# Kernel optimization log

Hardware: AMD Instinct MI355X
Metric: run time of the kernel (lower is better)

Reference implementation:

```python
import jax, jax.numpy as jnp
import numpy as np

N = 100_000      # nodes
E = 1_600_000    # edges (avg degree 16)
IN_DIM = 128
HID = 512
NCLS = 64
BN_EPS = 1e-5


def setup_inputs() -> dict:
    key = jax.random.key(0)
    ks = jax.random.split(key, 16)

    def lin(k, fi, fo):
        kw, kb = jax.random.split(k)
        s = 1.0 / np.sqrt(fi)
        return (jax.random.uniform(kw, (fi, fo), jnp.float32, -s, s),
                jax.random.uniform(kb, (fo,), jnp.float32, -s, s))

    W1a, b1a = lin(ks[2], IN_DIM, HID)
    W1b, b1b = lin(ks[3], HID, HID)
    W2a, b2a = lin(ks[4], HID, HID)
    W2b, b2b = lin(ks[5], HID, NCLS)
    return {
        "x": jax.random.normal(ks[0], (N, IN_DIM), jnp.float32),
        "edge_index": jax.random.randint(ks[1], (2, E), 0, N, jnp.int32),
        "g": jnp.zeros((1,), jnp.int32),
        "A_k": jnp.zeros((1,), jnp.int32),
        "D": jnp.zeros((1,), jnp.int32),
        "Kindices": jnp.zeros((1,), jnp.int32),
        "de": jnp.zeros((1,), jnp.int32),
        "M": jnp.zeros((1,), jnp.int32),
        "I": jnp.zeros((1,), jnp.int32),
        "W1a": W1a, "b1a": b1a, "W1b": W1b, "b1b": b1b,
        "gamma1": jnp.ones((HID,), jnp.float32), "beta1": jnp.zeros((HID,), jnp.float32),
        "W2a": W2a, "b2a": b2a, "W2b": W2b, "b2b": b2b,
        "gamma2": jnp.ones((NCLS,), jnp.float32), "beta2": jnp.zeros((NCLS,), jnp.float32),
    }


def _gin_conv(x, src, dst, Wa, ba, Wb, bb):
    # PyG GINConv (eps=0): nn(x + sum_{j in N(i)} x_j); messages x[src] summed at dst
    agg = jax.ops.segment_sum(x[src], dst, num_segments=N)
    h = x + agg
    h = jax.nn.relu(h @ Wa + ba)
    return h @ Wb + bb


def _batchnorm(x, gamma, beta):
    # training-mode BatchNorm1d: batch stats over node dim, biased variance
    mu = jnp.mean(x, axis=0)
    var = jnp.mean(jnp.square(x - mu), axis=0)
    return gamma * (x - mu) * jax.lax.rsqrt(var + BN_EPS) + beta


def reference(x, edge_index, g, A_k, D, Kindices, de, M, I,
              W1a, b1a, W1b, b1b, gamma1, beta1,
              W2a, b2a, W2b, b2b, gamma2, beta2):
    src, dst = edge_index[0], edge_index[1]
    h = jax.nn.selu(_gin_conv(x, src, dst, W1a, b1a, W1b, b1b))
    h = _batchnorm(h, gamma1, beta1)
    # dropout(p=0.5) omitted (eval-mode / deterministic reference)
    h = jax.nn.selu(_gin_conv(h, src, dst, W2a, b2a, W2b, b2b))
    h = _batchnorm(h, gamma2, beta2)
    return jax.nn.softmax(h, axis=1)
```

## Files before the change

kernel.cpp:

```cpp
#include <hip/hip_runtime.h>
#include <hip/hip_bf16.h>

#define N_NODES 100000
#define N_EDGES 1600000
#define IN_DIM 128
#define HID 512
#define NCLS 64

typedef __attribute__((ext_vector_type(8))) short bf16x8;
typedef __attribute__((ext_vector_type(4))) float f32x4;

#define RB_COUNT 782
#define RB_PAD 784
#define TG_GRID (RB_PAD * 4)

__device__ inline float bf2f(unsigned short b) {
    unsigned int u = ((unsigned int)b) << 16;
    return __builtin_bit_cast(float, u);
}
__device__ inline unsigned short f2bf(float f) {
    unsigned int u = __builtin_bit_cast(unsigned int, f);
    unsigned int lsb = (u >> 16) & 1u;
    u += 0x7fffu + lsb;
    return (unsigned short)(u >> 16);
}
__device__ inline float selu_f(float x) {
    const float scale = 1.0507009873554805f;
    const float alpha = 1.6732632423543772f;
    return x > 0.f ? scale * x : scale * alpha * (__expf(x) - 1.f);
}
__device__ inline void stb(float* p, float v) { *p = v; }
__device__ inline void stb(unsigned short* p, float v) { *p = f2bf(v); }

__device__ inline void gl_lds16(const void* g, void* l) {
    __builtin_amdgcn_global_load_lds((const __attribute__((address_space(1))) void*)g,
                                     (__attribute__((address_space(3))) void*)l, 16, 0, 0);
}

__global__ __launch_bounds__(256) void k_cast(const float* __restrict__ x,
                                              unsigned short* __restrict__ xb) {
    size_t g = (size_t)blockIdx.x * 256 + threadIdx.x;
    size_t total = (size_t)N_NODES * IN_DIM / 8;
    if (g >= total) return;
    const float4* p = (const float4*)(x + g * 8);
    float4 v0 = p[0], v1 = p[1];
    uint4 o;
    o.x = (unsigned)f2bf(v0.x) | ((unsigned)f2bf(v0.y) << 16);
    o.y = (unsigned)f2bf(v0.z) | ((unsigned)f2bf(v0.w) << 16);
    o.z = (unsigned)f2bf(v1.x) | ((unsigned)f2bf(v1.y) << 16);
    o.w = (unsigned)f2bf(v1.z) | ((unsigned)f2bf(v1.w) << 16);
    ((uint4*)xb)[g] = o;
}

__global__ __launch_bounds__(256) void k_deg(const int* __restrict__ dst, int* __restrict__ deg) {
    int e = blockIdx.x * 256 + threadIdx.x;
    if (e < N_EDGES) atomicAdd(&deg[dst[e]], 1);
}

#define SCAN_NB 98

__global__ __launch_bounds__(256) void k_scan_part(const int* __restrict__ deg, int* __restrict__ part) {
    __shared__ int sd[256];
    int b = blockIdx.x, t = threadIdx.x;
    int i0 = b * 1024 + t * 4;
    int s = 0;
#pragma unroll
    for (int k = 0; k < 4; ++k) if (i0 + k < N_NODES) s += deg[i0 + k];
    sd[t] = s;
    __syncthreads();
    for (int o = 128; o > 0; o >>= 1) {
        if (t < o) sd[t] += sd[t + o];
        __syncthreads();
    }
    if (t == 0) part[b] = sd[0];
}

__global__ __launch_bounds__(128) void k_scan_mid(const int* __restrict__ part, int* __restrict__ base,
                                                  int* __restrict__ off) {
    __shared__ int sp[128];
    int t = threadIdx.x;
    int v = (t < SCAN_NB) ? part[t] : 0;
    sp[t] = v;
    __syncthreads();
    for (int o = 1; o < 128; o <<= 1) {
        int tv = (t >= o) ? sp[t - o] : 0;
        __syncthreads();
        sp[t] += tv;
        __syncthreads();
    }
    if (t < SCAN_NB) base[t] = sp[t] - v;
    if (t == SCAN_NB - 1) off[N_NODES] = sp[t];
}

__global__ __launch_bounds__(256) void k_scan_fin(const int* __restrict__ deg, const int* __restrict__ base,
                                                  int* __restrict__ off, int* __restrict__ pos) {
    __shared__ int sd[256];
    int b = blockIdx.x, t = threadIdx.x;
    int i0 = b * 1024 + t * 4;
    int v[4]; int s = 0;
#pragma unroll
    for (int k = 0; k < 4; ++k) { v[k] = (i0 + k < N_NODES) ? deg[i0 + k] : 0; s += v[k]; }
    sd[t] = s;
    __syncthreads();
    for (int o = 1; o < 256; o <<= 1) {
        int tv = (t >= o) ? sd[t - o] : 0;
        __syncthreads();
        sd[t] += tv;
        __syncthreads();
    }
    int excl = base[b] + sd[t] - s;
#pragma unroll
    for (int k = 0; k < 4; ++k) {
        if (i0 + k < N_NODES) { off[i0 + k] = excl; pos[i0 + k] = excl; excl += v[k]; }
    }
}

__global__ __launch_bounds__(256) void k_fill(const int* __restrict__ src, const int* __restrict__ dst,
                                              int* __restrict__ pos, int* __restrict__ adj) {
    int e = blockIdx.x * 256 + threadIdx.x;
    if (e < N_EDGES) {
        int p = atomicAdd(&pos[dst[e]], 1);
        adj[p] = src[e];
    }
}

__global__ __launch_bounds__(256) void k_sortadj(const int* __restrict__ off, int* __restrict__ adj) {
    __shared__ int sb[64 * 256];
    int n = blockIdx.x * 256 + threadIdx.x;
    if (n >= N_NODES) return;
    int t = threadIdx.x;
    int e0 = off[n], e1 = off[n + 1];
    int d = e1 - e0;
    if (d <= 1 || d > 64) return;
    for (int i = 0; i < d; ++i) sb[i * 256 + t] = adj[e0 + i];
    for (int i = 1; i < d; ++i) {
        int key = sb[i * 256 + t];
        int j = i - 1;
        while (j >= 0 && sb[j * 256 + t] > key) {
            sb[(j + 1) * 256 + t] = sb[j * 256 + t];
            --j;
        }
        sb[(j + 1) * 256 + t] = key;
    }
    for (int i = 0; i < d; ++i) adj[e0 + i] = sb[i * 256 + t];
}

__global__ __launch_bounds__(256) void k_pack(const float* __restrict__ W,
                                              unsigned short* __restrict__ Wp, int K, int NC) {
    int idx = blockIdx.x * 256 + threadIdx.x;
    if (idx >= K * NC) return;
    int j = idx & 7;
    int l = (idx >> 3) & 63;
    int t = idx >> 9;
    int KT = K >> 5;
    int kt = t % KT;
    int nt = t / KT;
    int k = kt * 32 + (l >> 4) * 8 + j;
    int n = nt * 16 + (l & 15);
    Wp[idx] = f2bf(W[(size_t)k * NC + n]);
}

__global__ __launch_bounds__(256) void k_packT(const float* __restrict__ W,
                                               unsigned short* __restrict__ WT, int K, int NC) {
    int idx = blockIdx.x * 256 + threadIdx.x;
    if (idx >= K * NC) return;
    int k = idx & (K - 1);
    int n = idx / K;
    WT[idx] = f2bf(W[(size_t)k * NC + n]);
}

__global__ __launch_bounds__(256) void k_agg1(const unsigned short* __restrict__ xb,
                                              const int* __restrict__ off, const int* __restrict__ adj,
                                              unsigned short* __restrict__ A1) {
    int w = (blockIdx.x * 256 + threadIdx.x) >> 6;
    if (w >= N_NODES) return;
    int lane = threadIdx.x & 63;
    unsigned v = ((const unsigned*)(xb + (size_t)w * IN_DIM))[lane];
    float s0 = bf2f((unsigned short)(v & 0xffff));
    float s1 = bf2f((unsigned short)(v >> 16));
    int e0 = off[w], e1 = off[w + 1];
    int e = e0;
    for (; e + 4 <= e1; e += 4) {
        int j0 = adj[e], j1 = adj[e + 1], j2 = adj[e + 2], j3 = adj[e + 3];
        unsigned u0 = ((const unsigned*)(xb + (size_t)j0 * IN_DIM))[lane];
        unsigned u1 = ((const unsigned*)(xb + (size_t)j1 * IN_DIM))[lane];
        unsigned u2 = ((const unsigned*)(xb + (size_t)j2 * IN_DIM))[lane];
        unsigned u3 = ((const unsigned*)(xb + (size_t)j3 * IN_DIM))[lane];
        s0 += bf2f((unsigned short)(u0 & 0xffff)) + bf2f((unsigned short)(u1 & 0xffff)) +
              bf2f((unsigned short)(u2 & 0xffff)) + bf2f((unsigned short)(u3 & 0xffff));
        s1 += bf2f((unsigned short)(u0 >> 16)) + bf2f((unsigned short)(u1 >> 16)) +
              bf2f((unsigned short)(u2 >> 16)) + bf2f((unsigned short)(u3 >> 16));
    }
    for (; e < e1; ++e) {
        unsigned u = ((const unsigned*)(xb + (size_t)adj[e] * IN_DIM))[lane];
        s0 += bf2f((unsigned short)(u & 0xffff));
        s1 += bf2f((unsigned short)(u >> 16));
    }
    ((unsigned*)(A1 + (size_t)w * IN_DIM))[lane] = (unsigned)f2bf(s0) | ((unsigned)f2bf(s1) << 16);
}

__global__ __launch_bounds__(256) void k_aggbn2(const unsigned short* __restrict__ h,
                                                const int* __restrict__ off, const int* __restrict__ adj,
                                                const float* __restrict__ bn,
                                                unsigned short* __restrict__ outb) {
    int w = (blockIdx.x * 256 + threadIdx.x) >> 6;
    if (w >= N_NODES) return;
    int lane = threadIdx.x & 63;
    int fb = blockIdx.y * 256 + lane * 4;
    const unsigned short* hp = h + fb;
    float scl[4], shf[4];
#pragma unroll
    for (int k = 0; k < 4; ++k) {
        scl[k] = bn[2 * HID + fb + k];
        shf[k] = bn[3 * HID + fb + k];
    }
    uint2 v = *(const uint2*)(hp + (size_t)w * HID);
    float s0 = bf2f((unsigned short)(v.x & 0xffff));
    float s1 = bf2f((unsigned short)(v.x >> 16));
    float s2 = bf2f((unsigned short)(v.y & 0xffff));
    float s3 = bf2f((unsigned short)(v.y >> 16));
    int e0 = off[w], e1 = off[w + 1];
    int e = e0;
    for (; e + 4 <= e1; e += 4) {
        int j0 = adj[e], j1 = adj[e + 1], j2 = adj[e + 2], j3 = adj[e + 3];
        uint2 u0 = *(const uint2*)(hp + (size_t)j0 * HID);
        uint2 u1 = *(const uint2*)(hp + (size_t)j1 * HID);
        uint2 u2 = *(const uint2*)(hp + (size_t)j2 * HID);
        uint2 u3 = *(const uint2*)(hp + (size_t)j3 * HID);
        s0 += bf2f((unsigned short)(u0.x & 0xffff)) + bf2f((unsigned short)(u1.x & 0xffff)) +
              bf2f((unsigned short)(u2.x & 0xffff)) + bf2f((unsigned short)(u3.x & 0xffff));
        s1 += bf2f((unsigned short)(u0.x >> 16)) + bf2f((unsigned short)(u1.x >> 16)) +
              bf2f((unsigned short)(u2.x >> 16)) + bf2f((unsigned short)(u3.x >> 16));
        s2 += bf2f((unsigned short)(u0.y & 0xffff)) + bf2f((unsigned short)(u1.y & 0xffff)) +
              bf2f((unsigned short)(u2.y & 0xffff)) + bf2f((unsigned short)(u3.y & 0xffff));
        s3 += bf2f((unsigned short)(u0.y >> 16)) + bf2f((unsigned short)(u1.y >> 16)) +
              bf2f((unsigned short)(u2.y >> 16)) + bf2f((unsigned short)(u3.y >> 16));
    }
    for (; e < e1; ++e) {
        uint2 u = *(const uint2*)(hp + (size_t)adj[e] * HID);
        s0 += bf2f((unsigned short)(u.x & 0xffff));
        s1 += bf2f((unsigned short)(u.x >> 16));
        s2 += bf2f((unsigned short)(u.y & 0xffff));
        s3 += bf2f((unsigned short)(u.y >> 16));
    }
    float dp1 = (float)(e1 - e0 + 1);
    float r0 = s0 * scl[0] + dp1 * shf[0];
    float r1 = s1 * scl[1] + dp1 * shf[1];
    float r2 = s2 * scl[2] + dp1 * shf[2];
    float r3 = s3 * scl[3] + dp1 * shf[3];
    unsigned long long o =
        (unsigned long long)((unsigned)f2bf(r0) | ((unsigned)f2bf(r1) << 16)) |
        ((unsigned long long)((unsigned)f2bf(r2) | ((unsigned)f2bf(r3) << 16)) << 32);
    __builtin_nontemporal_store(o, (unsigned long long*)(outb + (size_t)w * HID + fb));
}

template <int K, int ACT, int STATS>
__global__ __launch_bounds__(256) void k_tgemm(const unsigned short* __restrict__ A,
                                               const unsigned short* __restrict__ WT,
                                               const float* __restrict__ bias,
                                               unsigned short* __restrict__ Out,
                                               float* __restrict__ scratch, int M) {
    constexpr int NC = 512;
    __shared__ __align__(16) char smem[32768 + 2048];
    const int bid = blockIdx.x;
    const int r8 = bid & 7;
    const int q = bid >> 3;
    const int cb = q & 3;
    const int rb = (q >> 2) * 8 + r8;
    const int rowbase = rb * 128;
    const int colbase = cb * 128;
    if (rowbase >= M) return;

    const int tid = threadIdx.x;
    const int lane = tid & 63;
    const int w = tid >> 6;
    const int wm = w >> 1, wn = w & 1;
    const int l15 = lane & 15, lg = lane >> 4;

    f32x4 acc[4][4];
#pragma unroll
    for (int i = 0; i < 4; ++i)
#pragma unroll
        for (int j = 0; j < 4; ++j) acc[i][j] = (f32x4)0.f;

    for (int k0 = 0; k0 < K; k0 += 64) {
#pragma unroll
        for (int i = 0; i < 4; ++i) {
            int slot = i * 256 + tid;
            int r = slot >> 3;
            int u = (slot & 7) ^ (r & 7);
            int gr = rowbase + r; if (gr >= M) gr = M - 1;
            gl_lds16(A + (size_t)gr * K + k0 + u * 8, smem + (i * 256 + w * 64) * 16);
        }
#pragma unroll
        for (int i = 0; i < 4; ++i) {
            int slot = i * 256 + tid;
            int c = slot >> 3;
            int u = (slot & 7) ^ (c & 7);
            gl_lds16(WT + (size_t)(colbase + c) * K + k0 + u * 8,
                     smem + 16384 + (i * 256 + w * 64) * 16);
        }
        __syncthreads();
#pragma unroll
        for (int kin = 0; kin < 2; ++kin) {
            bf16x8 af[4], bfr[4];
#pragma unroll
            for (int mi = 0; mi < 4; ++mi) {
                int r = wm * 64 + mi * 16 + l15;
                int u = (kin * 4 + lg) ^ (r & 7);
                af[mi] = *(const bf16x8*)(smem + r * 128 + u * 16);
            }
#pragma unroll
            for (int ni = 0; ni < 4; ++ni) {
                int c = wn * 64 + ni * 16 + l15;
                int u = (kin * 4 + lg) ^ (c & 7);
                bfr[ni] = *(const bf16x8*)(smem + 16384 + c * 128 + u * 16);
            }
#pragma unroll
            for (int mi = 0; mi < 4; ++mi)
#pragma unroll
                for (int ni = 0; ni < 4; ++ni)
                    acc[mi][ni] = __builtin_amdgcn_mfma_f32_16x16x32_bf16(af[mi], bfr[ni], acc[mi][ni], 0, 0, 0);
        }
        __syncthreads();
    }

    float cs[4], cq[4];
    if (STATS) {
#pragma unroll
        for (int ni = 0; ni < 4; ++ni) { cs[ni] = 0.f; cq[ni] = 0.f; }
    }
#pragma unroll
    for (int ni = 0; ni < 4; ++ni) {
        int c = wn * 64 + ni * 16 + l15;
        float bv = bias[colbase + c];
#pragma unroll
        for (int mi = 0; mi < 4; ++mi) {
#pragma unroll
            for (int r = 0; r < 4; ++r) {
                int row = wm * 64 + mi * 16 + lg * 4 + r;
                float t = acc[mi][ni][r] + bv;
                t = (ACT == 0) ? fmaxf(t, 0.f) : selu_f(t);
                if (STATS && (rowbase + row < M)) { cs[ni] += t; cq[ni] += t * t; }
                int byte = (row * 256 + c * 2) ^ ((row & 7) << 4);
                *(unsigned short*)(smem + byte) = f2bf(t);
            }
        }
    }
    if (STATS) {
        float* sS = (float*)(smem + 32768);
#pragma unroll
        for (int ni = 0; ni < 4; ++ni) {
            float a = cs[ni];
            a += __shfl_xor(a, 16); a += __shfl_xor(a, 32);
            float b = cq[ni];
            b += __shfl_xor(b, 16); b += __shfl_xor(b, 32);
            if (lg == 0) {
                sS[wm * 256 + (wn * 64 + ni * 16 + l15)] = a;
                sS[wm * 256 + 128 + (wn * 64 + ni * 16 + l15)] = b;
            }
        }
    }
    __syncthreads();
#pragma unroll
    for (int it = 0; it < 8; ++it) {
        int idx = it * 256 + tid;
        int row = idx >> 4;
        int ch = idx & 15;
        int gr = rowbase + row;
        if (gr < M) {
            uint4 v = *(const uint4*)(smem + row * 256 + ((ch ^ (row & 7)) << 4));
            *(uint4*)(Out + (size_t)gr * NC + colbase + ch * 8) = v;
        }
    }
    if (STATS) {
        const float* sS = (const float*)(smem + 32768);
        int c = tid & 127, kind = tid >> 7;
        float v = sS[kind * 128 + c] + sS[256 + kind * 128 + c];
        scratch[(size_t)(rb * 4 + cb) * 256 + kind * 128 + c] = v;
    }
}

__global__ __launch_bounds__(256) void k_bnred(const float* __restrict__ scratch,
                                               float* __restrict__ bn) {
    int t = threadIdx.x;
    float loc[4] = {0.f, 0.f, 0.f, 0.f};
    for (int rb = blockIdx.x; rb < RB_COUNT; rb += gridDim.x) {
#pragma unroll
        for (int cbk = 0; cbk < 4; ++cbk)
            loc[cbk] += scratch[(size_t)(rb * 4 + cbk) * 256 + t];
    }
    int kind = t >> 7, cl = t & 127;
#pragma unroll
    for (int cbk = 0; cbk < 4; ++cbk)
        atomicAdd(&bn[kind * HID + cbk * 128 + cl], loc[cbk]);
}

template <int K, int NC, int ACT, int WAVES_M, int WAVES_N, int NFRAG, int STATS, typename TOUT>
__global__ __launch_bounds__(WAVES_M * WAVES_N * 64) void k_mgemm(
    const unsigned short* __restrict__ A, const unsigned short* __restrict__ Wp,
    const float* __restrict__ bias, TOUT* __restrict__ Out, float* __restrict__ bnacc, int M) {
    __shared__ float sS[WAVES_M * WAVES_N * 128];
    const int tid = threadIdx.x;
    const int lane = tid & 63;
    const int w = tid >> 6;
    const int wm = w / WAVES_N;
    const int wn = w % WAVES_N;
    const int l15 = lane & 15;
    const int lg = lane >> 4;
    const int rowbase = blockIdx.x * (32 * WAVES_M) + wm * 32;
    const int colbase = blockIdx.y * (WAVES_N * 16 * NFRAG) + wn * 16 * NFRAG;
    int r0 = rowbase + l15; if (r0 > M - 1) r0 = M - 1;
    int r1 = rowbase + 16 + l15; if (r1 > M - 1) r1 = M - 1;
    const unsigned short* pa0 = A + (size_t)r0 * K + lg * 8;
    const unsigned short* pa1 = A + (size_t)r1 * K + lg * 8;
    const unsigned short* pw = Wp + (size_t)(colbase >> 4) * (K / 32) * 512 + lane * 8;

    f32x4 acc[2][NFRAG];
#pragma unroll
    for (int i = 0; i < 2; ++i)
#pragma unroll
        for (int j = 0; j < NFRAG; ++j) acc[i][j] = (f32x4)0.f;

#pragma unroll 2
    for (int kt = 0; kt < K / 32; ++kt) {
        bf16x8 a0 = *(const bf16x8*)(pa0 + kt * 32);
        bf16x8 a1 = *(const bf16x8*)(pa1 + kt * 32);
#pragma unroll
        for (int ni = 0; ni < NFRAG; ++ni) {
            bf16x8 bv = *(const bf16x8*)(pw + (ni * (K / 32) + kt) * 512);
            acc[0][ni] = __builtin_amdgcn_mfma_f32_16x16x32_bf16(a0, bv, acc[0][ni], 0, 0, 0);
            acc[1][ni] = __builtin_amdgcn_mfma_f32_16x16x32_bf16(a1, bv, acc[1][ni], 0, 0, 0);
        }
    }

    float cs[NFRAG], cq[NFRAG];
    if (STATS) {
#pragma unroll
        for (int ni = 0; ni < NFRAG; ++ni) { cs[ni] = 0.f; cq[ni] = 0.f; }
    }
#pragma unroll
    for (int ni = 0; ni < NFRAG; ++ni) {
        int c = colbase + ni * 16 + l15;
        float bv = bias[c];
#pragma unroll
        for (int mi = 0; mi < 2; ++mi) {
#pragma unroll
            for (int r = 0; r < 4; ++r) {
                int row = rowbase + mi * 16 + lg * 4 + r;
                if (row < M) {
                    float t = acc[mi][ni][r] + bv;
                    t = (ACT == 0) ? fmaxf(t, 0.f) : selu_f(t);
                    if (STATS) { cs[ni] += t; cq[ni] += t * t; }
                    stb(&Out[(size_t)row * NC + c], t);
                }
            }
        }
    }
    if (STATS) {
#pragma unroll
        for (int ni = 0; ni < NFRAG; ++ni) {
            float a = cs[ni];
            a += __shfl_xor(a, 16); a += __shfl_xor(a, 32);
            float b = cq[ni];
            b += __shfl_xor(b, 16); b += __shfl_xor(b, 32);
            if (lg == 0) {
                sS[w * 128 + (ni * 16 + l15)] = a;
                sS[w * 128 + 64 + (ni * 16 + l15)] = b;
            }
        }
        __syncthreads();
        if (tid < 128) {
            float v = 0.f;
#pragma unroll
            for (int ww = 0; ww < WAVES_M * WAVES_N; ++ww) v += sS[ww * 128 + tid];
            atomicAdd(&bnacc[tid], v);
        }
    }
}

__global__ void k_bnprep(float* __restrict__ bn, const float* __restrict__ gamma,
                         const float* __restrict__ beta, int C, float invn) {
    int c = threadIdx.x + blockIdx.x * blockDim.x;
    if (c >= C) return;
    float mu = bn[c] * invn;
    float var = bn[C + c] * invn - mu * mu;
    float sc = gamma[c] * rsqrtf(var + 1e-5f);
    bn[2 * C + c] = sc;
    bn[3 * C + c] = beta[c] - mu * sc;
}

__global__ __launch_bounds__(256) void k_softmax(float* __restrict__ O, const float* __restrict__ bn2) {
    int w = (blockIdx.x * 256 + threadIdx.x) >> 6;
    if (w >= N_NODES) return;
    int lane = threadIdx.x & 63;
    float z = O[(size_t)w * NCLS + lane] * bn2[2 * NCLS + lane] + bn2[3 * NCLS + lane];
    float m = z;
#pragma unroll
    for (int o = 32; o > 0; o >>= 1) m = fmaxf(m, __shfl_xor(m, o));
    float e = __expf(z - m);
    float s = e;
#pragma unroll
    for (int o = 32; o > 0; o >>= 1) s += __shfl_xor(s, o);
    O[(size_t)w * NCLS + lane] = e / s;
}

extern "C" void kernel_launch(void* const* d_in, const int* in_sizes, int n_in,
                              void* d_out, int out_size, void* d_ws, size_t ws_size,
                              hipStream_t stream) {
    const float* x = (const float*)d_in[0];
    const int* edge = (const int*)d_in[1];
    const int* srcp = edge;
    const int* dstp = edge + N_EDGES;
    const float* W1a = (const float*)d_in[9];
    const float* b1a = (const float*)d_in[10];
    const float* W1b = (const float*)d_in[11];
    const float* b1b = (const float*)d_in[12];
    const float* gamma1 = (const float*)d_in[13];
    const float* beta1 = (const float*)d_in[14];
    const float* W2a = (const float*)d_in[15];
    const float* b2a = (const float*)d_in[16];
    const float* W2b = (const float*)d_in[17];
    const float* b2b = (const float*)d_in[18];
    const float* gamma2 = (const float*)d_in[19];
    const float* beta2 = (const float*)d_in[20];
    float* out = (float*)d_out;

    char* ws = (char*)d_ws;
    size_t o = 0;
    auto alloc = [&](size_t bytes) -> char* {
        char* p = ws + o;
        o = (o + bytes + 255) & ~(size_t)255;
        return p;
    };
    int* off = (int*)alloc((N_NODES + 1) * sizeof(int));
    int* deg = (int*)alloc(N_NODES * sizeof(int));
    int* pos = (int*)alloc(N_NODES * sizeof(int));
    int* adj = (int*)alloc(N_EDGES * sizeof(int));
    int* part = (int*)alloc(SCAN_NB * sizeof(int));
    int* base = (int*)alloc(SCAN_NB * sizeof(int));
    float* bn1 = (float*)alloc(4 * HID * sizeof(float));
    float* bn2 = (float*)alloc(4 * NCLS * sizeof(float));
    float* stat = (float*)alloc((size_t)RB_COUNT * 4 * 256 * sizeof(float));
    unsigned short* WT1 = (unsigned short*)alloc((size_t)IN_DIM * HID * sizeof(unsigned short));
    unsigned short* WT2 = (unsigned short*)alloc((size_t)HID * HID * sizeof(unsigned short));
    unsigned short* WT3 = (unsigned short*)alloc((size_t)HID * HID * sizeof(unsigned short));
    unsigned short* Wp4 = (unsigned short*)alloc((size_t)HID * NCLS * sizeof(unsigned short));
    unsigned short* xb = (unsigned short*)alloc((size_t)N_NODES * IN_DIM * sizeof(unsigned short));
    unsigned short* A1 = (unsigned short*)alloc((size_t)N_NODES * IN_DIM * sizeof(unsigned short));
    unsigned short* B = (unsigned short*)alloc((size_t)N_NODES * HID * sizeof(unsigned short));
    unsigned short* C = (unsigned short*)alloc((size_t)N_NODES * HID * sizeof(unsigned short));

    hipMemsetAsync(deg, 0, N_NODES * sizeof(int), stream);
    hipMemsetAsync(bn1, 0, 2 * HID * sizeof(float), stream);
    hipMemsetAsync(bn2, 0, 2 * NCLS * sizeof(float), stream);

    int eb = (N_EDGES + 255) / 256;
    k_cast<<<(N_NODES * IN_DIM / 8 + 255) / 256, 256, 0, stream>>>(x, xb);
    k_deg<<<eb, 256, 0, stream>>>(dstp, deg);
    k_scan_part<<<SCAN_NB, 256, 0, stream>>>(deg, part);
    k_scan_mid<<<1, 128, 0, stream>>>(part, base, off);
    k_scan_fin<<<SCAN_NB, 256, 0, stream>>>(deg, base, off, pos);
    k_fill<<<eb, 256, 0, stream>>>(srcp, dstp, pos, adj);
    k_sortadj<<<(N_NODES + 255) / 256, 256, 0, stream>>>(off, adj);

    k_packT<<<(IN_DIM * HID) / 256, 256, 0, stream>>>(W1a, WT1, IN_DIM, HID);
    k_packT<<<(HID * HID) / 256, 256, 0, stream>>>(W1b, WT2, HID, HID);
    k_packT<<<(HID * HID) / 256, 256, 0, stream>>>(W2a, WT3, HID, HID);
    k_pack<<<(HID * NCLS) / 256, 256, 0, stream>>>(W2b, Wp4, HID, NCLS);

    int nwb = (N_NODES * 64 + 255) / 256;

    k_agg1<<<nwb, 256, 0, stream>>>(xb, off, adj, A1);
    k_tgemm<IN_DIM, 0, 0><<<TG_GRID, 256, 0, stream>>>(A1, WT1, b1a, B, nullptr, N_NODES);
    k_tgemm<HID, 1, 1><<<TG_GRID, 256, 0, stream>>>(B, WT2, b1b, C, stat, N_NODES);
    k_bnred<<<32, 256, 0, stream>>>(stat, bn1);
    k_bnprep<<<2, 256, 0, stream>>>(bn1, gamma1, beta1, HID, 1.0f / N_NODES);

    k_aggbn2<<<dim3(nwb, 2), 256, 0, stream>>>(C, off, adj, bn1, B);
    k_tgemm<HID, 0, 0><<<TG_GRID, 256, 0, stream>>>(B, WT3, b2a, C, nullptr, N_NODES);
    k_mgemm<HID, NCLS, 1, 8, 1, 4, 1, float><<<dim3((N_NODES + 255) / 256, 1), 512, 0, stream>>>(C, Wp4, b2b, out, bn2, N_NODES);

    k_bnprep<<<1, 64, 0, stream>>>(bn2, gamma2, beta2, NCLS, 1.0f / N_NODES);
    k_softmax<<<nwb, 256, 0, stream>>>(out, bn2);
}
```

Measured before the change: 881.5 us.

## Split layer-2 aggregation into eight feature slices with edge-parallel lanes

The second-layer gather/BN kernel now handles 64-feature slices across eight sequential launches, with each wavefront's four 16-lane groups splitting a node's edges and reducing through cross-lane shuffles. The intent is to shrink the gathered working set per launch (100k nodes × 64 features in bf16) so that it fits in cache, raising hit rates on the random neighbour reads. The cost is eight launches instead of one, eight re-reads of the CSR offsets and adjacency, and shuffle reductions. Each gather is also narrower (8 bytes per lane across 16 lanes, so 128-byte segments).

After: 1.114 ms. +26.4%, slower.

```diff
diff --git a/kernel.cpp b/kernel.cpp
--- a/kernel.cpp
+++ b/kernel.cpp
@@ -199,59 +199,60 @@
     ((unsigned*)(A1 + (size_t)w * IN_DIM))[lane] = (unsigned)f2bf(s0) | ((unsigned)f2bf(s1) << 16);
 }
 
-__global__ __launch_bounds__(256) void k_aggbn2(const unsigned short* __restrict__ h,
+__global__ __launch_bounds__(256) void k_aggbn8(const unsigned short* __restrict__ h,
                                                 const int* __restrict__ off, const int* __restrict__ adj,
                                                 const float* __restrict__ bn,
-                                                unsigned short* __restrict__ outb) {
+                                                unsigned short* __restrict__ outb, int slice) {
     int w = (blockIdx.x * 256 + threadIdx.x) >> 6;
     if (w >= N_NODES) return;
     int lane = threadIdx.x & 63;
-    int fb = blockIdx.y * 256 + lane * 4;
+    int es = lane >> 4;
+    int fl = lane & 15;
+    int fb = slice * 64 + fl * 4;
     const unsigned short* hp = h + fb;
-    float scl[4], shf[4];
-#pragma unroll
-    for (int k = 0; k < 4; ++k) {
-        scl[k] = bn[2 * HID + fb + k];
-        shf[k] = bn[3 * HID + fb + k];
-    }
-    uint2 v = *(const uint2*)(hp + (size_t)w * HID);
-    float s0 = bf2f((unsigned short)(v.x & 0xffff));
-    float s1 = bf2f((unsigned short)(v.x >> 16));
-    float s2 = bf2f((unsigned short)(v.y & 0xffff));
-    float s3 = bf2f((unsigned short)(v.y >> 16));
+    float s0 = 0.f, s1 = 0.f, s2 = 0.f, s3 = 0.f;
+    if (es == 0) {
+        unsigned long long sv = __builtin_nontemporal_load(
+            (const unsigned long long*)(hp + (size_t)w * HID));
+        s0 = bf2f((unsigned short)(sv & 0xffff));
+        s1 = bf2f((unsigned short)((sv >> 16) & 0xffff));
+        s2 = bf2f((unsigned short)((sv >> 32) & 0xffff));
+        s3 = bf2f((unsigned short)((sv >> 48) & 0xffff));
+    }
     int e0 = off[w], e1 = off[w + 1];
-    int e = e0;
-    for (; e + 4 <= e1; e += 4) {
-        int j0 = adj[e], j1 = adj[e + 1], j2 = adj[e + 2], j3 = adj[e + 3];
-        uint2 u0 = *(const uint2*)(hp + (size_t)j0 * HID);
-        uint2 u1 = *(const uint2*)(hp + (size_t)j1 * HID);
-        uint2 u2 = *(const uint2*)(hp + (size_t)j2 * HID);
-        uint2 u3 = *(const uint2*)(hp + (size_t)j3 * HID);
-        s0 += bf2f((unsigned short)(u0.x & 0xffff)) + bf2f((unsigned short)(u1.x & 0xffff)) +
-              bf2f((unsigned short)(u2.x & 0xffff)) + bf2f((unsigned short)(u3.x & 0xffff));
-        s1 += bf2f((unsigned short)(u0.x >> 16)) + bf2f((unsigned short)(u1.x >> 16)) +
-              bf2f((unsigned short)(u2.x >> 16)) + bf2f((unsigned short)(u3.x >> 16));
-        s2 += bf2f((unsigned short)(u0.y & 0xffff)) + bf2f((unsigned short)(u1.y & 0xffff)) +
-              bf2f((unsigned short)(u2.y & 0xffff)) + bf2f((unsigned short)(u3.y & 0xffff));
-        s3 += bf2f((unsigned short)(u0.y >> 16)) + bf2f((unsigned short)(u1.y >> 16)) +
-              bf2f((unsigned short)(u2.y >> 16)) + bf2f((unsigned short)(u3.y >> 16));
-    }
-    for (; e < e1; ++e) {
-        uint2 u = *(const uint2*)(hp + (size_t)adj[e] * HID);
+    int e = e0 + es;
+    for (; e + 4 < e1; e += 8) {
+        int ja = adj[e], jb = adj[e + 4];
+        uint2 ua = *(const uint2*)(hp + (size_t)ja * HID);
+        uint2 ub = *(const uint2*)(hp + (size_t)jb * HID);
+        s0 += bf2f((unsigned short)(ua.x & 0xffff)) + bf2f((unsigned short)(ub.x & 0xffff));
+        s1 += bf2f((unsigned short)(ua.x >> 16)) + bf2f((unsigned short)(ub.x >> 16));
+        s2 += bf2f((unsigned short)(ua.y & 0xffff)) + bf2f((unsigned short)(ub.y & 0xffff));
+        s3 += bf2f((unsigned short)(ua.y >> 16)) + bf2f((unsigned short)(ub.y >> 16));
+    }
+    for (; e < e1; e += 4) {
+        int j = adj[e];
+        uint2 u = *(const uint2*)(hp + (size_t)j * HID);
         s0 += bf2f((unsigned short)(u.x & 0xffff));
         s1 += bf2f((unsigned short)(u.x >> 16));
         s2 += bf2f((unsigned short)(u.y & 0xffff));
         s3 += bf2f((unsigned short)(u.y >> 16));
     }
-    float dp1 = (float)(e1 - e0 + 1);
-    float r0 = s0 * scl[0] + dp1 * shf[0];
-    float r1 = s1 * scl[1] + dp1 * shf[1];
-    float r2 = s2 * scl[2] + dp1 * shf[2];
-    float r3 = s3 * scl[3] + dp1 * shf[3];
-    unsigned long long o =
-        (unsigned long long)((unsigned)f2bf(r0) | ((unsigned)f2bf(r1) << 16)) |
-        ((unsigned long long)((unsigned)f2bf(r2) | ((unsigned)f2bf(r3) << 16)) << 32);
-    __builtin_nontemporal_store(o, (unsigned long long*)(outb + (size_t)w * HID + fb));
+    s0 += __shfl_xor(s0, 16); s0 += __shfl_xor(s0, 32);
+    s1 += __shfl_xor(s1, 16); s1 += __shfl_xor(s1, 32);
+    s2 += __shfl_xor(s2, 16); s2 += __shfl_xor(s2, 32);
+    s3 += __shfl_xor(s3, 16); s3 += __shfl_xor(s3, 32);
+    if (es == 0) {
+        float dp1 = (float)(e1 - e0 + 1);
+        float r0 = s0 * bn[2 * HID + fb + 0] + dp1 * bn[3 * HID + fb + 0];
+        float r1 = s1 * bn[2 * HID + fb + 1] + dp1 * bn[3 * HID + fb + 1];
+        float r2 = s2 * bn[2 * HID + fb + 2] + dp1 * bn[3 * HID + fb + 2];
+        float r3 = s3 * bn[2 * HID + fb + 3] + dp1 * bn[3 * HID + fb + 3];
+        unsigned long long o =
+            (unsigned long long)((unsigned)f2bf(r0) | ((unsigned)f2bf(r1) << 16)) |
+            ((unsigned long long)((unsigned)f2bf(r2) | ((unsigned)f2bf(r3) << 16)) << 32);
+        __builtin_nontemporal_store(o, (unsigned long long*)(outb + (size_t)w * HID + fb));
+    }
 }
 
 template <int K, int ACT, int STATS>
@@ -577,8 +578,10 @@
     k_bnred<<<32, 256, 0, stream>>>(stat, bn1);
     k_bnprep<<<2, 256, 0, stream>>>(bn1, gamma1, beta1, HID, 1.0f / N_NODES);
 
-    k_aggbn2<<<dim3(nwb, 2), 256, 0, stream>>>(C, off, adj, bn1, B);
-    k_tgemm<HID, 0, 0><<<TG_GRID, 256, 0, stream>>>(B, WT3, b2a, C, nullptr, N_NODES);
+    for (int sl = 0; sl < 8; ++sl)
+        k_aggbn8<<<nwb, 256, 0, stream>>>(C, off, adj, bn1, B, sl);
+
+    k_tgemm<HID, 0, 0><<<TG_GRID, 256, 0, stream>>>(B, WT3, b2a, C, N_NODES ? nullptr : nullptr, N_NODES);
     k_mgemm<HID, NCLS, 1, 8, 1, 4, 1, float><<<dim3((N_NODES + 255) / 256, 1), 512, 0, stream>>>(C, Wp4, b2b, out, bn2, N_NODES);
 
     k_bnprep<<<1, 64, 0, stream>>>(bn2, gamma2, beta2, NCLS, 1.0f / N_NODES);
```

## Load GEMM weights directly from pre-packed MFMA layout instead of LDS staging

Applied to the files above, without the earlier changes.

The three 512-column GEMMs now read weight fragments straight from global memory in a pre-packed per-lane MFMA layout (k_pack), instead of staging a transposed weight tile through LDS. LDS use is halved, and the epilogue writes the output in two 64-row passes so it fits in the smaller buffer. This removes the weight LDS copy and may raise occupancy. In exchange, each wave issues global or L2 loads for B fragments inside the K loop, which adds latency and redundant traffic across waves, plus extra barriers in the epilogue.

Result: slower. 949.4 us (+7.7%).

```diff
diff --git a/kernel.cpp b/kernel.cpp
--- a/kernel.cpp
+++ b/kernel.cpp
@@ -158,15 +158,6 @@
     int k = kt * 32 + (l >> 4) * 8 + j;
     int n = nt * 16 + (l & 15);
     Wp[idx] = f2bf(W[(size_t)k * NC + n]);
-}
-
-__global__ __launch_bounds__(256) void k_packT(const float* __restrict__ W,
-                                               unsigned short* __restrict__ WT, int K, int NC) {
-    int idx = blockIdx.x * 256 + threadIdx.x;
-    if (idx >= K * NC) return;
-    int k = idx & (K - 1);
-    int n = idx / K;
-    WT[idx] = f2bf(W[(size_t)k * NC + n]);
 }
 
 __global__ __launch_bounds__(256) void k_agg1(const unsigned short* __restrict__ xb,
@@ -255,13 +246,14 @@
 }
 
 template <int K, int ACT, int STATS>
-__global__ __launch_bounds__(256) void k_tgemm(const unsigned short* __restrict__ A,
-                                               const unsigned short* __restrict__ WT,
+__global__ __launch_bounds__(256) void k_hgemm(const unsigned short* __restrict__ A,
+                                               const unsigned short* __restrict__ Wp,
                                                const float* __restrict__ bias,
                                                unsigned short* __restrict__ Out,
                                                float* __restrict__ scratch, int M) {
     constexpr int NC = 512;
-    __shared__ __align__(16) char smem[32768 + 2048];
+    constexpr int KT = K / 32;
+    __shared__ __align__(16) char smem[16384 + 2048];
     const int bid = blockIdx.x;
     const int r8 = bid & 7;
     const int q = bid >> 3;
@@ -276,6 +268,8 @@
     const int w = tid >> 6;
     const int wm = w >> 1, wn = w & 1;
     const int l15 = lane & 15, lg = lane >> 4;
+    const int ntbase = (colbase >> 4) + wn * 4;
+    const unsigned short* pwb = Wp + (size_t)lane * 8;
 
     f32x4 acc[4][4];
 #pragma unroll
@@ -292,18 +286,11 @@
             int gr = rowbase + r; if (gr >= M) gr = M - 1;
             gl_lds16(A + (size_t)gr * K + k0 + u * 8, smem + (i * 256 + w * 64) * 16);
         }
-#pragma unroll
-        for (int i = 0; i < 4; ++i) {
-            int slot = i * 256 + tid;
-            int c = slot >> 3;
-            int u = (slot & 7) ^ (c & 7);
-            gl_lds16(WT + (size_t)(colbase + c) * K + k0 + u * 8,
-                     smem + 16384 + (i * 256 + w * 64) * 16);
-        }
         __syncthreads();
 #pragma unroll
         for (int kin = 0; kin < 2; ++kin) {
-            bf16x8 af[4], bfr[4];
+            int kt = (k0 >> 5) + kin;
+            bf16x8 af[4], bv[4];
 #pragma unroll
             for (int mi = 0; mi < 4; ++mi) {
                 int r = wm * 64 + mi * 16 + l15;
@@ -311,44 +298,59 @@
                 af[mi] = *(const bf16x8*)(smem + r * 128 + u * 16);
             }
 #pragma unroll
+            for (int ni = 0; ni < 4; ++ni)
+                bv[ni] = *(const bf16x8*)(pwb + (size_t)((ntbase + ni) * KT + kt) * 512);
+#pragma unroll
+            for (int ni = 0; ni < 4; ++ni)
+#pragma unroll
+                for (int mi = 0; mi < 4; ++mi)
+                    acc[mi][ni] = __builtin_amdgcn_mfma_f32_16x16x32_bf16(af[mi], bv[ni], acc[mi][ni], 0, 0, 0);
+        }
+        __syncthreads();
+    }
+
+    float cs[4], cq[4];
+    if (STATS) {
+#pragma unroll
+        for (int ni = 0; ni < 4; ++ni) { cs[ni] = 0.f; cq[ni] = 0.f; }
+    }
+#pragma unroll
+    for (int pass = 0; pass < 2; ++pass) {
+        if (wm == pass) {
+#pragma unroll
             for (int ni = 0; ni < 4; ++ni) {
                 int c = wn * 64 + ni * 16 + l15;
-                int u = (kin * 4 + lg) ^ (c & 7);
-                bfr[ni] = *(const bf16x8*)(smem + 16384 + c * 128 + u * 16);
+                float bvs = bias[colbase + c];
+#pragma unroll
+                for (int mi = 0; mi < 4; ++mi) {
+#pragma unroll
+                    for (int r = 0; r < 4; ++r) {
+                        int rloc = mi * 16 + lg * 4 + r;
+                        float t = acc[mi][ni][r] + bvs;
+                        t = (ACT == 0) ? fmaxf(t, 0.f) : selu_f(t);
+                        if (STATS && (rowbase + pass * 64 + rloc < M)) { cs[ni] += t; cq[ni] += t * t; }
+                        int byte = (rloc * 256 + c * 2) ^ ((rloc & 7) << 4);
+                        *(unsigned short*)(smem + byte) = f2bf(t);
+                    }
+                }
             }
-#pragma unroll
-            for (int mi = 0; mi < 4; ++mi)
-#pragma unroll
-                for (int ni = 0; ni < 4; ++ni)
-                    acc[mi][ni] = __builtin_amdgcn_mfma_f32_16x16x32_bf16(af[mi], bfr[ni], acc[mi][ni], 0, 0, 0);
-        }
-        __syncthreads();
-    }
-
-    float cs[4], cq[4];
+        }
+        __syncthreads();
+#pragma unroll
+        for (int it = 0; it < 4; ++it) {
+            int idx = it * 256 + tid;
+            int row = idx >> 4;
+            int ch = idx & 15;
+            int gr = rowbase + pass * 64 + row;
+            if (gr < M) {
+                uint4 v = *(const uint4*)(smem + row * 256 + ((ch ^ (row & 7)) << 4));
+                *(uint4*)(Out + (size_t)gr * NC + colbase + ch * 8) = v;
+            }
+        }
+        __syncthreads();
+    }
     if (STATS) {
-#pragma unroll
-        for (int ni = 0; ni < 4; ++ni) { cs[ni] = 0.f; cq[ni] = 0.f; }
-    }
-#pragma unroll
-    for (int ni = 0; ni < 4; ++ni) {
-        int c = wn * 64 + ni * 16 + l15;
-        float bv = bias[colbase + c];
-#pragma unroll
-        for (int mi = 0; mi < 4; ++mi) {
-#pragma unroll
-            for (int r = 0; r < 4; ++r) {
-                int row = wm * 64 + mi * 16 + lg * 4 + r;
-                float t = acc[mi][ni][r] + bv;
-                t = (ACT == 0) ? fmaxf(t, 0.f) : selu_f(t);
-                if (STATS && (rowbase + row < M)) { cs[ni] += t; cq[ni] += t * t; }
-                int byte = (row * 256 + c * 2) ^ ((row & 7) << 4);
-                *(unsigned short*)(smem + byte) = f2bf(t);
-            }
-        }
-    }
-    if (STATS) {
-        float* sS = (float*)(smem + 32768);
+        float* sS = (float*)(smem + 16384);
 #pragma unroll
         for (int ni = 0; ni < 4; ++ni) {
             float a = cs[ni];
@@ -360,24 +362,12 @@
                 sS[wm * 256 + 128 + (wn * 64 + ni * 16 + l15)] = b;
             }
         }
-    }
-    __syncthreads();
-#pragma unroll
-    for (int it = 0; it < 8; ++it) {
-        int idx = it * 256 + tid;
-        int row = idx >> 4;
-        int ch = idx & 15;
-        int gr = rowbase + row;
-        if (gr < M) {
-            uint4 v = *(const uint4*)(smem + row * 256 + ((ch ^ (row & 7)) << 4));
-            *(uint4*)(Out + (size_t)gr * NC + colbase + ch * 8) = v;
-        }
-    }
-    if (STATS) {
-        const float* sS = (const float*)(smem + 32768);
+        __syncthreads();
         int c = tid & 127, kind = tid >> 7;
-        float v = sS[kind * 128 + c] + sS[256 + kind * 128 + c];
-        scratch[(size_t)(rb * 4 + cb) * 256 + kind * 128 + c] = v;
+        if (tid < 256) {
+            float v = sS[kind * 128 + c] + sS[256 + kind * 128 + c];
+            scratch[(size_t)(rb * 4 + cb) * 256 + kind * 128 + c] = v;
+        }
     }
 }
 
@@ -542,9 +532,9 @@
     float* bn1 = (float*)alloc(4 * HID * sizeof(float));
     float* bn2 = (float*)alloc(4 * NCLS * sizeof(float));
     float* stat = (float*)alloc((size_t)RB_COUNT * 4 * 256 * sizeof(float));
-    unsigned short* WT1 = (unsigned short*)alloc((size_t)IN_DIM * HID * sizeof(unsigned short));
-    unsigned short* WT2 = (unsigned short*)alloc((size_t)HID * HID * sizeof(unsigned short));
-    unsigned short* WT3 = (unsigned short*)alloc((size_t)HID * HID * sizeof(unsigned short));
+    unsigned short* Wp1 = (unsigned short*)alloc((size_t)IN_DIM * HID * sizeof(unsigned short));
+    unsigned short* Wp2 = (unsigned short*)alloc((size_t)HID * HID * sizeof(unsigned short));
+    unsigned short* Wp3 = (unsigned short*)alloc((size_t)HID * HID * sizeof(unsigned short));
     unsigned short* Wp4 = (unsigned short*)alloc((size_t)HID * NCLS * sizeof(unsigned short));
     unsigned short* xb = (unsigned short*)alloc((size_t)N_NODES * IN_DIM * sizeof(unsigned short));
     unsigned short* A1 = (unsigned short*)alloc((size_t)N_NODES * IN_DIM * sizeof(unsigned short));
@@ -564,21 +554,21 @@
     k_fill<<<eb, 256, 0, stream>>>(srcp, dstp, pos, adj);
     k_sortadj<<<(N_NODES + 255) / 256, 256, 0, stream>>>(off, adj);
 
-    k_packT<<<(IN_DIM * HID) / 256, 256, 0, stream>>>(W1a, WT1, IN_DIM, HID);
-    k_packT<<<(HID * HID) / 256, 256, 0, stream>>>(W1b, WT2, HID, HID);
-    k_packT<<<(HID * HID) / 256, 256, 0, stream>>>(W2a, WT3, HID, HID);
+    k_pack<<<(IN_DIM * HID) / 256, 256, 0, stream>>>(W1a, Wp1, IN_DIM, HID);
+    k_pack<<<(HID * HID) / 256, 256, 0, stream>>>(W1b, Wp2, HID, HID);
+    k_pack<<<(HID * HID) / 256, 256, 0, stream>>>(W2a, Wp3, HID, HID);
     k_pack<<<(HID * NCLS) / 256, 256, 0, stream>>>(W2b, Wp4, HID, NCLS);
 
     int nwb = (N_NODES * 64 + 255) / 256;
 
     k_agg1<<<nwb, 256, 0, stream>>>(xb, off, adj, A1);
-    k_tgemm<IN_DIM, 0, 0><<<TG_GRID, 256, 0, stream>>>(A1, WT1, b1a, B, nullptr, N_NODES);
-    k_tgemm<HID, 1, 1><<<TG_GRID, 256, 0, stream>>>(B, WT2, b1b, C, stat, N_NODES);
+    k_hgemm<IN_DIM, 0, 0><<<TG_GRID, 256, 0, stream>>>(A1, Wp1, b1a, B, nullptr, N_NODES);
+    k_hgemm<HID, 1, 1><<<TG_GRID, 256, 0, stream>>>(B, Wp2, b1b, C, stat, N_NODES);
     k_bnred<<<32, 256, 0, stream>>>(stat, bn1);
     k_bnprep<<<2, 256, 0, stream>>>(bn1, gamma1, beta1, HID, 1.0f / N_NODES);
 
     k_aggbn2<<<dim3(nwb, 2), 256, 0, stream>>>(C, off, adj, bn1, B);
-    k_tgemm<HID, 0, 0><<<TG_GRID, 256, 0, stream>>>(B, WT3, b2a, C, nullptr, N_NODES);
+    k_hgemm<HID, 0, 0><<<TG_GRID, 256, 0, stream>>>(B, Wp3, b2a, C, nullptr, N_NODES);
     k_mgemm<HID, NCLS, 1, 8, 1, 4, 1, float><<<dim3((N_NODES + 255) / 256, 1), 512, 0, stream>>>(C, Wp4, b2b, out, bn2, N_NODES);
 
     k_bnprep<<<1, 64, 0, stream>>>(bn2, gamma2, beta2, NCLS, 1.0f / N_NODES);
```
